# Kernel optimization log

Hardware: AMD Instinct MI355X
Metric: run time of the kernel (lower is better)

Reference implementation:

```python
import jax, jax.numpy as jnp
import numpy as np

B, T, D = 8, 2048, 512
F = 512          # filters (== D due to residual add)
K = 7            # kernel_size
H = 128          # hidden_dim of kernel generator (hard-coded in source)
LN_EPS = 1e-3    # keras LayerNormalization default epsilon


def setup_inputs() -> dict:
    key = jax.random.key(0)
    ks = jax.random.split(key, 8)
    x = jax.random.normal(ks[0], (B, T, D), dtype=jnp.float32)
    # kernel generator: Dense(D->H, relu) then Dense(H->K*F)
    W1 = jax.random.normal(ks[1], (D, H), dtype=jnp.float32) * (1.0 / np.sqrt(D))
    b1 = jnp.zeros((H,), dtype=jnp.float32)
    W2 = jax.random.normal(ks[2], (H, K * F), dtype=jnp.float32) * (1.0 / np.sqrt(H))
    b2 = jnp.zeros((K * F,), dtype=jnp.float32)
    # LayerNorm params
    gamma = jnp.ones((F,), dtype=jnp.float32)
    beta = jnp.zeros((F,), dtype=jnp.float32)
    return {"x": x, "W1": W1, "b1": b1, "W2": W2, "b2": b2,
            "gamma": gamma, "beta": beta}


def _dynamic_conv_block(x, W1, b1, W2, b2, gamma, beta):
    # per-token dynamic kernels: [B, T, K, F]
    h = jax.nn.relu(jnp.einsum("btd,dh->bth", x, W1) + b1)
    kernels = (jnp.einsum("bth,hf->btf", h, W2) + b2).reshape(B, T, K, F)
    # extract sliding-window patches (same padding): [B, T, K, D]
    pad = K // 2
    xp = jnp.pad(x, ((0, 0), (pad, pad), (0, 0)))
    patches = jnp.stack([xp[:, i:i + T, :] for i in range(K)], axis=2)
    # per-token conv: contract over window K and input channels D
    conv_out = jnp.einsum("btkd,btkf->btf", patches, kernels)
    # residual + LayerNorm + relu (dropout is identity at inference)
    y = conv_out + x
    mu = jnp.mean(y, axis=-1, keepdims=True)
    var = jnp.mean(jnp.square(y - mu), axis=-1, keepdims=True)
    y = (y - mu) * jax.lax.rsqrt(var + LN_EPS) * gamma + beta
    return jax.nn.relu(y)


def reference(x, W1, b1, W2, b2, gamma, beta):
    return _dynamic_conv_block(x, W1, b1, W2, b2, gamma, beta)
```

## Files before the change

kernel.cpp:

```cpp
#include <hip/hip_runtime.h>

#define NB 8
#define NT 2048
#define ND 512
#define NH 128
#define NF 512
#define NKW 7
#define NTOK (NB*NT)
#define KP 960

typedef float f32x4 __attribute__((ext_vector_type(4)));
typedef __bf16 bf16x8 __attribute__((ext_vector_type(8)));
typedef unsigned short u16;
typedef unsigned int u32;
typedef u16 u16x8 __attribute__((ext_vector_type(8)));

__device__ __forceinline__ u16 f2bf(float f){
  u32 u = __builtin_bit_cast(u32, f);
  return (u16)((u + 0x7fffu + ((u>>16)&1u)) >> 16);
}
__device__ __forceinline__ float bf2f(u16 s){
  u32 u = ((u32)s)<<16;
  return __builtin_bit_cast(float, u);
}
__device__ __forceinline__ void gload_lds16(const void* g, void* l){
  __builtin_amdgcn_global_load_lds(
      (const __attribute__((address_space(1))) void*)g,
      (__attribute__((address_space(3))) void*)l, 16, 0, 0);
}
__device__ __forceinline__ void store16_lds(void* p, const u16 u[8]){
  u32 d0 = (u32)u[0] | ((u32)u[1]<<16);
  u32 d1 = (u32)u[2] | ((u32)u[3]<<16);
  u32 d2 = (u32)u[4] | ((u32)u[5]<<16);
  u32 d3 = (u32)u[6] | ((u32)u[7]<<16);
  int4 vv; vv.x=(int)d0; vv.y=(int)d1; vv.z=(int)d2; vv.w=(int)d3;
  *(int4*)p = vv;
}

__global__ __launch_bounds__(256) void prep_kernel(
    const float* __restrict__ W1, const float* __restrict__ W2,
    const float* __restrict__ b2, u16* __restrict__ W1T, u16* __restrict__ B2T)
{
  int e = blockIdx.x*256 + threadIdx.x;
  if (e < ND*NH){
    int k = e >> 7, h = e & (NH-1);
    W1T[h*ND + k] = f2bf(W1[e]);
  } else if (e < ND*NH + NH*NKW*NF){
    int c = e - ND*NH;
    int h = c / (NKW*NF);
    int col = c - h*(NKW*NF);
    int k = col >> 9, n = col & (NF-1);
    B2T[(size_t)n*KP + k*NH + h] = f2bf(W2[c]);
  } else if (e < ND*NH + NH*NKW*NF + NF*64){
    int c = e - (ND*NH + NH*NKW*NF);
    int n = c >> 6, j = c & 63;
    B2T[(size_t)n*KP + 896 + j] = (j < NKW) ? f2bf(b2[j*NF + n]) : (u16)0;
  }
}

__global__ __launch_bounds__(256) void rowsum_kernel(
    const float* __restrict__ x, float* __restrict__ rs)
{
  int t = blockIdx.x*4 + (threadIdx.x>>6);
  int l = threadIdx.x & 63;
  const float4* p = (const float4*)(x + (size_t)t*ND + l*8);
  float4 a = p[0], b = p[1];
  float s = (a.x+a.y)+(a.z+a.w)+((b.x+b.y)+(b.z+b.w));
  #pragma unroll
  for (int m=1;m<64;m<<=1) s += __shfl_xor(s, m);
  if (l==0) rs[t] = s;
}

__global__ __launch_bounds__(256) void gemm1_kernel(
    const float* __restrict__ x, const u16* __restrict__ W1T,
    const float* __restrict__ b1, u16* __restrict__ hout)
{
  __shared__ __align__(16) u16 At[64*64];
  __shared__ __align__(16) u16 Bt[128*64];
  const int tid = threadIdx.x, w = tid>>6, l = tid&63;
  const int m_base = blockIdx.x*64;
  f32x4 acc[4][2] = {};
  for (int kc=0; kc<8; ++kc){
    if (kc) __syncthreads();
    #pragma unroll
    for (int it=0; it<2; ++it){
      int c = tid + it*256;
      int row = c>>3, slot = c&7;
      const float4* px = (const float4*)(x + (size_t)(m_base+row)*ND + kc*64 + slot*8);
      float4 a = px[0], b = px[1];
      u16 u[8] = {f2bf(a.x),f2bf(a.y),f2bf(a.z),f2bf(a.w),
                  f2bf(b.x),f2bf(b.y),f2bf(b.z),f2bf(b.w)};
      int byte = row*128 + ((slot*16) ^ ((row&7)<<4));
      store16_lds((char*)At + byte, u);
    }
    #pragma unroll
    for (int i=0;i<4;++i){
      int rowbase = i*32 + w*8;
      char* ldsbase = (char*)Bt + rowbase*128;
      int n = rowbase + (l>>3);
      const char* g = (const char*)W1T + (size_t)n*1024 + kc*128
                      + (((l&7)*16) ^ (((l>>3)&7)<<4));
      gload_lds16(g, ldsbase);
    }
    asm volatile("s_waitcnt vmcnt(0)" ::: "memory");
    __syncthreads();
    #pragma unroll
    for (int kk=0; kk<2; ++kk){
      bf16x8 af[4], bfr[2];
      #pragma unroll
      for (int mi=0;mi<4;++mi){
        int row = mi*16 + (l&15);
        int byte = row*128 + (((kk*64)+((l>>4)*16)) ^ ((row&7)<<4));
        af[mi] = *(const bf16x8*)((const char*)At + byte);
      }
      #pragma unroll
      for (int ni=0;ni<2;++ni){
        int row = w*32 + ni*16 + (l&15);
        int byte = row*128 + (((kk*64)+((l>>4)*16)) ^ ((row&7)<<4));
        bfr[ni] = *(const bf16x8*)((const char*)Bt + byte);
      }
      #pragma unroll
      for (int mi=0;mi<4;++mi)
        #pragma unroll
        for (int ni=0;ni<2;++ni)
          acc[mi][ni] = __builtin_amdgcn_mfma_f32_16x16x32_bf16(af[mi], bfr[ni], acc[mi][ni], 0,0,0);
    }
  }
  #pragma unroll
  for (int ni=0;ni<2;++ni){
    int n = w*32 + ni*16 + (l&15);
    float bias = b1[n];
    #pragma unroll
    for (int mi=0;mi<4;++mi){
      #pragma unroll
      for (int r=0;r<4;++r){
        int m = mi*16 + (l>>4)*4 + r;
        float v = fmaxf(acc[mi][ni][r] + bias, 0.f);
        hout[(size_t)(m_base+m)*NH + n] = f2bf(v);
      }
    }
  }
}

__global__ __launch_bounds__(512) void gemm2_kernel(
    const float* __restrict__ x, const u16* __restrict__ hbuf,
    const u16* __restrict__ B2T, const float* __restrict__ rs,
    const float* __restrict__ gamma, const float* __restrict__ beta,
    float* __restrict__ out)
{
  __shared__ __align__(16) u16 At[64*64];
  __shared__ __align__(16) u16 Bt[512*64];
  __shared__ float s_lds[64][8];
  __shared__ float g_lds[512], be_lds[512];
  __shared__ float red_s[64][8], red_q[64][8];
  __shared__ float mu_lds[64], rstd_lds[64];

  const int tid = threadIdx.x, w = tid>>6, l = tid&63;
  const int m_base = blockIdx.x*64;

  g_lds[tid] = gamma[tid];
  be_lds[tid] = beta[tid];
  {
    int row = tid>>3, k = tid&7;
    float v = 0.f;
    if (k < NKW){
      int tg = m_base + row;
      int ti = tg & (NT-1);
      int idx = ti + k - 3;
      if (idx >= 0 && idx < NT) v = rs[(tg & ~(NT-1)) + idx];
    }
    s_lds[row][k] = v;
  }

  f32x4 acc[4][4] = {};
  for (int kc=0; kc<15; ++kc){
    __syncthreads();
    {
      int row = tid>>3, slot = tid&7;
      u16 u[8];
      if (kc < 14){
        float sv = s_lds[row][kc>>1];
        u16x8 hv = *(const u16x8*)(hbuf + (size_t)(m_base+row)*NH + (kc&1)*64 + slot*8);
        #pragma unroll
        for (int j=0;j<8;++j) u[j] = f2bf(bf2f(hv[j])*sv);
      } else {
        #pragma unroll
        for (int j=0;j<8;++j){
          int e2 = slot*8+j;
          float v = (e2<NKW)? s_lds[row][e2] : 0.f;
          u[j] = f2bf(v);
        }
      }
      int byte = row*128 + ((slot*16) ^ ((row&7)<<4));
      store16_lds((char*)At + byte, u);
    }
    #pragma unroll
    for (int i=0;i<8;++i){
      int rowbase = i*64 + w*8;
      char* ldsbase = (char*)Bt + rowbase*128;
      int n = rowbase + (l>>3);
      const char* g = (const char*)B2T + (size_t)n*(KP*2) + kc*128
                      + (((l&7)*16) ^ (((l>>3)&7)<<4));
      gload_lds16(g, ldsbase);
    }
    asm volatile("s_waitcnt vmcnt(0)" ::: "memory");
    __syncthreads();
    #pragma unroll
    for (int kk=0; kk<2; ++kk){
      bf16x8 af[4], bfr[4];
      #pragma unroll
      for (int mi=0;mi<4;++mi){
        int row = mi*16 + (l&15);
        int byte = row*128 + (((kk*64)+((l>>4)*16)) ^ ((row&7)<<4));
        af[mi] = *(const bf16x8*)((const char*)At + byte);
      }
      #pragma unroll
      for (int ni=0;ni<4;++ni){
        int row = w*64 + ni*16 + (l&15);
        int byte = row*128 + (((kk*64)+((l>>4)*16)) ^ ((row&7)<<4));
        bfr[ni] = *(const bf16x8*)((const char*)Bt + byte);
      }
      #pragma unroll
      for (int mi=0;mi<4;++mi)
        #pragma unroll
        for (int ni=0;ni<4;++ni)
          acc[mi][ni] = __builtin_amdgcn_mfma_f32_16x16x32_bf16(af[mi], bfr[ni], acc[mi][ni], 0,0,0);
    }
  }
  #pragma unroll
  for (int mi=0;mi<4;++mi){
    #pragma unroll
    for (int r=0;r<4;++r){
      int m = mi*16 + (l>>4)*4 + r;
      int tg = m_base + m;
      float ps=0.f, pq=0.f;
      #pragma unroll
      for (int ni=0;ni<4;++ni){
        int n = w*64 + ni*16 + (l&15);
        float v = acc[mi][ni][r] + x[(size_t)tg*ND + n];
        acc[mi][ni][r] = v;
        ps += v; pq += v*v;
      }
      #pragma unroll
      for (int msk=1; msk<16; msk<<=1){ ps += __shfl_xor(ps,msk); pq += __shfl_xor(pq,msk); }
      if ((l&15)==0){ red_s[m][w]=ps; red_q[m][w]=pq; }
    }
  }
  __syncthreads();
  if (tid < 64){
    float ssum=0.f, sq=0.f;
    #pragma unroll
    for (int ww=0; ww<8; ++ww){ ssum += red_s[tid][ww]; sq += red_q[tid][ww]; }
    float mu = ssum * (1.0f/ND);
    float var = sq*(1.0f/ND) - mu*mu;
    mu_lds[tid] = mu;
    rstd_lds[tid] = rsqrtf(var + 1e-3f);
  }
  __syncthreads();
  #pragma unroll
  for (int mi=0;mi<4;++mi){
    #pragma unroll
    for (int r=0;r<4;++r){
      int m = mi*16 + (l>>4)*4 + r;
      int tg = m_base + m;
      float mu = mu_lds[m], rstd = rstd_lds[m];
      #pragma unroll
      for (int ni=0;ni<4;++ni){
        int n = w*64 + ni*16 + (l&15);
        float v = (acc[mi][ni][r]-mu)*rstd*g_lds[n] + be_lds[n];
        out[(size_t)tg*ND + n] = fmaxf(v, 0.f);
      }
    }
  }
}

extern "C" void kernel_launch(void* const* d_in, const int* in_sizes, int n_in,
                              void* d_out, int out_size, void* d_ws, size_t ws_size,
                              hipStream_t stream)
{
  (void)in_sizes; (void)n_in; (void)out_size; (void)ws_size;
  const float* x     = (const float*)d_in[0];
  const float* W1    = (const float*)d_in[1];
  const float* b1    = (const float*)d_in[2];
  const float* W2    = (const float*)d_in[3];
  const float* b2    = (const float*)d_in[4];
  const float* gamma = (const float*)d_in[5];
  const float* beta  = (const float*)d_in[6];
  float* out = (float*)d_out;

  char* ws = (char*)d_ws;
  u16*   W1T  = (u16*)(ws);
  u16*   B2T  = (u16*)(ws + 131072);
  float* rs   = (float*)(ws + 131072 + 983040);
  u16*   hbuf = (u16*)(ws + 131072 + 983040 + 65536);

  prep_kernel<<<2176, 256, 0, stream>>>(W1, W2, b2, W1T, B2T);
  rowsum_kernel<<<NTOK/4, 256, 0, stream>>>(x, rs);
  gemm1_kernel<<<NTOK/64, 256, 0, stream>>>(x, W1T, b1, hbuf);
  gemm2_kernel<<<NTOK/64, 512, 0, stream>>>(x, hbuf, B2T, rs, gamma, beta, out);
}
```

Baseline: 148.2 us.

## Fuse rowsum into gemm1, register-prefetch B operands, double-buffer A tiles

```diff
diff --git a/kernel.cpp b/kernel.cpp
--- a/kernel.cpp
+++ b/kernel.cpp
@@ -1,12 +1,9 @@
 #include <hip/hip_runtime.h>
 
-#define NB 8
 #define NT 2048
 #define ND 512
 #define NH 128
-#define NF 512
 #define NKW 7
-#define NTOK (NB*NT)
 #define KP 960
 
 typedef float f32x4 __attribute__((ext_vector_type(4)));
@@ -22,11 +19,6 @@
 __device__ __forceinline__ float bf2f(u16 s){
   u32 u = ((u32)s)<<16;
   return __builtin_bit_cast(float, u);
-}
-__device__ __forceinline__ void gload_lds16(const void* g, void* l){
-  __builtin_amdgcn_global_load_lds(
-      (const __attribute__((address_space(1))) void*)g,
-      (__attribute__((address_space(3))) void*)l, 16, 0, 0);
 }
 __device__ __forceinline__ void store16_lds(void* p, const u16 u[8]){
   u32 d0 = (u32)u[0] | ((u32)u[1]<<16);
@@ -41,97 +33,136 @@
     const float* __restrict__ W1, const float* __restrict__ W2,
     const float* __restrict__ b2, u16* __restrict__ W1T, u16* __restrict__ B2T)
 {
-  int e = blockIdx.x*256 + threadIdx.x;
-  if (e < ND*NH){
-    int k = e >> 7, h = e & (NH-1);
-    W1T[h*ND + k] = f2bf(W1[e]);
-  } else if (e < ND*NH + NH*NKW*NF){
-    int c = e - ND*NH;
-    int h = c / (NKW*NF);
-    int col = c - h*(NKW*NF);
-    int k = col >> 9, n = col & (NF-1);
-    B2T[(size_t)n*KP + k*NH + h] = f2bf(W2[c]);
-  } else if (e < ND*NH + NH*NKW*NF + NF*64){
-    int c = e - (ND*NH + NH*NKW*NF);
-    int n = c >> 6, j = c & 63;
-    B2T[(size_t)n*KP + 896 + j] = (j < NKW) ? f2bf(b2[j*NF + n]) : (u16)0;
-  }
-}
-
-__global__ __launch_bounds__(256) void rowsum_kernel(
-    const float* __restrict__ x, float* __restrict__ rs)
+  __shared__ float T[64][65];
+  const int b = blockIdx.x, tid = threadIdx.x;
+  if (b < 16){
+    const int d0 = (b>>1)*64, h0 = (b&1)*64;
+    #pragma unroll
+    for (int r=0;r<16;++r){
+      int idx=r*256+tid; int dl=idx>>6, hl=idx&63;
+      T[dl][hl] = W1[(size_t)(d0+dl)*NH + h0+hl];
+    }
+    __syncthreads();
+    #pragma unroll
+    for (int r=0;r<16;++r){
+      int idx=r*256+tid; int hl=idx>>6, dl=idx&63;
+      W1T[(size_t)(h0+hl)*ND + d0+dl] = f2bf(T[dl][hl]);
+    }
+  } else if (b < 128){
+    const int bb = b-16;
+    const int h0 = (bb&1)*64, c0 = (bb>>1)*64;
+    #pragma unroll
+    for (int r=0;r<16;++r){
+      int idx=r*256+tid; int hl=idx>>6, cl=idx&63;
+      T[hl][cl] = W2[(size_t)(h0+hl)*(NKW*ND) + c0+cl];
+    }
+    __syncthreads();
+    #pragma unroll
+    for (int r=0;r<16;++r){
+      int idx=r*256+tid; int cl=idx>>6, hl=idx&63;
+      int c = c0+cl; int n = c & (ND-1), k = c >> 9;
+      B2T[(size_t)n*KP + k*NH + h0+hl] = f2bf(T[hl][cl]);
+    }
+  } else {
+    const int bb = b-128;
+    #pragma unroll
+    for (int r=0;r<16;++r){
+      int idx = bb*4096 + r*256 + tid;
+      int n = idx>>6, j = idx&63;
+      B2T[(size_t)n*KP + 896 + j] = (j<NKW)? f2bf(b2[(size_t)j*ND+n]) : (u16)0;
+    }
+  }
+}
+
+__device__ __forceinline__ void loadB2(const char* B2T, int kc, int w, int l,
+                                       bf16x8 (*bf)[4]){
+  #pragma unroll
+  for (int kk=0;kk<2;++kk)
+    #pragma unroll
+    for (int ni=0;ni<4;++ni){
+      int rowB = w*64 + ni*16 + (l&15);
+      bf[kk][ni] = *(const bf16x8*)(B2T + (size_t)rowB*(KP*2) + kc*128 + kk*64 + (l>>4)*16);
+    }
+}
+__device__ __forceinline__ void loadB1(const char* W1T, int kc, int w, int l,
+                                       bf16x8 (*bf)[2]){
+  #pragma unroll
+  for (int kk=0;kk<2;++kk)
+    #pragma unroll
+    for (int ni=0;ni<2;++ni){
+      int rowB = w*32 + ni*16 + (l&15);
+      bf[kk][ni] = *(const bf16x8*)(W1T + (size_t)rowB*(ND*2) + kc*128 + kk*64 + (l>>4)*16);
+    }
+}
+
+__global__ __launch_bounds__(256,2) void gemm1_kernel(
+    const float* __restrict__ x, const u16* __restrict__ W1T,
+    const float* __restrict__ b1, u16* __restrict__ hout, float* __restrict__ rs)
 {
-  int t = blockIdx.x*4 + (threadIdx.x>>6);
-  int l = threadIdx.x & 63;
-  const float4* p = (const float4*)(x + (size_t)t*ND + l*8);
-  float4 a = p[0], b = p[1];
-  float s = (a.x+a.y)+(a.z+a.w)+((b.x+b.y)+(b.z+b.w));
-  #pragma unroll
-  for (int m=1;m<64;m<<=1) s += __shfl_xor(s, m);
-  if (l==0) rs[t] = s;
-}
-
-__global__ __launch_bounds__(256) void gemm1_kernel(
-    const float* __restrict__ x, const u16* __restrict__ W1T,
-    const float* __restrict__ b1, u16* __restrict__ hout)
-{
-  __shared__ __align__(16) u16 At[64*64];
-  __shared__ __align__(16) u16 Bt[128*64];
+  __shared__ __align__(16) u16 At[2][32*64];
   const int tid = threadIdx.x, w = tid>>6, l = tid&63;
-  const int m_base = blockIdx.x*64;
-  f32x4 acc[4][2] = {};
-  for (int kc=0; kc<8; ++kc){
-    if (kc) __syncthreads();
-    #pragma unroll
-    for (int it=0; it<2; ++it){
-      int c = tid + it*256;
-      int row = c>>3, slot = c&7;
-      const float4* px = (const float4*)(x + (size_t)(m_base+row)*ND + kc*64 + slot*8);
-      float4 a = px[0], b = px[1];
-      u16 u[8] = {f2bf(a.x),f2bf(a.y),f2bf(a.z),f2bf(a.w),
-                  f2bf(b.x),f2bf(b.y),f2bf(b.z),f2bf(b.w)};
-      int byte = row*128 + ((slot*16) ^ ((row&7)<<4));
-      store16_lds((char*)At + byte, u);
-    }
-    #pragma unroll
-    for (int i=0;i<4;++i){
-      int rowbase = i*32 + w*8;
-      char* ldsbase = (char*)Bt + rowbase*128;
-      int n = rowbase + (l>>3);
-      const char* g = (const char*)W1T + (size_t)n*1024 + kc*128
-                      + (((l&7)*16) ^ (((l>>3)&7)<<4));
-      gload_lds16(g, ldsbase);
-    }
-    asm volatile("s_waitcnt vmcnt(0)" ::: "memory");
-    __syncthreads();
-    #pragma unroll
-    for (int kk=0; kk<2; ++kk){
-      bf16x8 af[4], bfr[2];
-      #pragma unroll
-      for (int mi=0;mi<4;++mi){
-        int row = mi*16 + (l&15);
-        int byte = row*128 + (((kk*64)+((l>>4)*16)) ^ ((row&7)<<4));
-        af[mi] = *(const bf16x8*)((const char*)At + byte);
-      }
-      #pragma unroll
-      for (int ni=0;ni<2;++ni){
-        int row = w*32 + ni*16 + (l&15);
-        int byte = row*128 + (((kk*64)+((l>>4)*16)) ^ ((row&7)<<4));
-        bfr[ni] = *(const bf16x8*)((const char*)Bt + byte);
-      }
-      #pragma unroll
-      for (int mi=0;mi<4;++mi)
+  const int m_base = blockIdx.x*32;
+  const int row = tid>>3, slot = tid&7;
+  const float* xrow = x + (size_t)(m_base+row)*ND + slot*8;
+  float rsum = 0.f;
+  f32x4 acc[2][2] = {};
+  bf16x8 bufA[2][2], bufB[2][2];
+
+  auto stageA = [&](u16* dst, const float4& p0, const float4& p1){
+    rsum += (p0.x+p0.y)+(p0.z+p0.w)+((p1.x+p1.y)+(p1.z+p1.w));
+    u16 u[8] = {f2bf(p0.x),f2bf(p0.y),f2bf(p0.z),f2bf(p0.w),
+                f2bf(p1.x),f2bf(p1.y),f2bf(p1.z),f2bf(p1.w)};
+    int byte = row*128 + ((slot*16) ^ ((row&7)<<4));
+    store16_lds((char*)dst + byte, u);
+  };
+
+  float4 c0 = *(const float4*)(xrow);
+  float4 c1 = *(const float4*)(xrow+4);
+  loadB1((const char*)W1T, 0, w, l, bufA);
+  stageA(At[0], c0, c1);
+  __syncthreads();
+
+  #pragma unroll
+  for (int kc=0;kc<8;++kc){
+    bf16x8 (*bc)[2] = (kc&1)? bufB : bufA;
+    bf16x8 (*bn)[2] = (kc&1)? bufA : bufB;
+    float4 n0, n1;
+    if (kc<7){
+      n0 = *(const float4*)(xrow + (kc+1)*64);
+      n1 = *(const float4*)(xrow + (kc+1)*64 + 4);
+      loadB1((const char*)W1T, kc+1, w, l, bn);
+    }
+    const char* curA = (const char*)At[kc&1];
+    #pragma unroll
+    for (int kk=0;kk<2;++kk){
+      bf16x8 af[2];
+      #pragma unroll
+      for (int mi=0;mi<2;++mi){
+        int r2 = mi*16 + (l&15);
+        int byte = r2*128 + (((kk*64)+((l>>4)*16)) ^ ((r2&7)<<4));
+        af[mi] = *(const bf16x8*)(curA + byte);
+      }
+      #pragma unroll
+      for (int mi=0;mi<2;++mi)
         #pragma unroll
         for (int ni=0;ni<2;++ni)
-          acc[mi][ni] = __builtin_amdgcn_mfma_f32_16x16x32_bf16(af[mi], bfr[ni], acc[mi][ni], 0,0,0);
-    }
-  }
+          acc[mi][ni] = __builtin_amdgcn_mfma_f32_16x16x32_bf16(af[mi], bc[kk][ni], acc[mi][ni],0,0,0);
+    }
+    if (kc<7){
+      stageA(At[(kc&1)^1], n0, n1);
+      __syncthreads();
+    }
+  }
+  rsum += __shfl_xor(rsum,1);
+  rsum += __shfl_xor(rsum,2);
+  rsum += __shfl_xor(rsum,4);
+  if ((tid&7)==0) rs[m_base+row] = rsum;
   #pragma unroll
   for (int ni=0;ni<2;++ni){
     int n = w*32 + ni*16 + (l&15);
     float bias = b1[n];
     #pragma unroll
-    for (int mi=0;mi<4;++mi){
+    for (int mi=0;mi<2;++mi){
       #pragma unroll
       for (int r=0;r<4;++r){
         int m = mi*16 + (l>>4)*4 + r;
@@ -142,91 +173,88 @@
   }
 }
 
-__global__ __launch_bounds__(512) void gemm2_kernel(
+__global__ __launch_bounds__(512,2) void gemm2_kernel(
     const float* __restrict__ x, const u16* __restrict__ hbuf,
     const u16* __restrict__ B2T, const float* __restrict__ rs,
     const float* __restrict__ gamma, const float* __restrict__ beta,
     float* __restrict__ out)
 {
-  __shared__ __align__(16) u16 At[64*64];
-  __shared__ __align__(16) u16 Bt[512*64];
+  __shared__ __align__(16) u16 At[2][64*64];
   __shared__ float s_lds[64][8];
-  __shared__ float g_lds[512], be_lds[512];
   __shared__ float red_s[64][8], red_q[64][8];
   __shared__ float mu_lds[64], rstd_lds[64];
 
   const int tid = threadIdx.x, w = tid>>6, l = tid&63;
   const int m_base = blockIdx.x*64;
-
-  g_lds[tid] = gamma[tid];
-  be_lds[tid] = beta[tid];
+  const int row = tid>>3, slot = tid&7;
+
   {
-    int row = tid>>3, k = tid&7;
+    int rr = tid>>3, k = tid&7;
     float v = 0.f;
     if (k < NKW){
-      int tg = m_base + row;
+      int tg = m_base + rr;
       int ti = tg & (NT-1);
       int idx = ti + k - 3;
       if (idx >= 0 && idx < NT) v = rs[(tg & ~(NT-1)) + idx];
     }
-    s_lds[row][k] = v;
-  }
+    s_lds[rr][k] = v;
+  }
+  u16x8 hv_e = *(const u16x8*)(hbuf + (size_t)(m_base+row)*NH + slot*8);
+  u16x8 hv_o = *(const u16x8*)(hbuf + (size_t)(m_base+row)*NH + 64 + slot*8);
+
+  bf16x8 bufA[2][4], bufB[2][4];
+  loadB2((const char*)B2T, 0, w, l, bufA);
+
+  auto stageA = [&](u16* dst, int kc2){
+    u16 u[8];
+    if (kc2 < 14){
+      float sv = s_lds[row][kc2>>1];
+      u16x8 hv = (kc2&1)? hv_o : hv_e;
+      #pragma unroll
+      for (int j=0;j<8;++j) u[j] = f2bf(bf2f(hv[j])*sv);
+    } else {
+      #pragma unroll
+      for (int j=0;j<8;++j){
+        int e2 = slot*8+j;
+        u[j] = (e2<NKW)? f2bf(s_lds[row][e2]) : (u16)0;
+      }
+    }
+    int byte = row*128 + ((slot*16) ^ ((row&7)<<4));
+    store16_lds((char*)dst + byte, u);
+  };
+
+  __syncthreads();
+  stageA(At[0], 0);
+  __syncthreads();
 
   f32x4 acc[4][4] = {};
-  for (int kc=0; kc<15; ++kc){
-    __syncthreads();
-    {
-      int row = tid>>3, slot = tid&7;
-      u16 u[8];
-      if (kc < 14){
-        float sv = s_lds[row][kc>>1];
-        u16x8 hv = *(const u16x8*)(hbuf + (size_t)(m_base+row)*NH + (kc&1)*64 + slot*8);
-        #pragma unroll
-        for (int j=0;j<8;++j) u[j] = f2bf(bf2f(hv[j])*sv);
-      } else {
-        #pragma unroll
-        for (int j=0;j<8;++j){
-          int e2 = slot*8+j;
-          float v = (e2<NKW)? s_lds[row][e2] : 0.f;
-          u[j] = f2bf(v);
-        }
-      }
-      int byte = row*128 + ((slot*16) ^ ((row&7)<<4));
-      store16_lds((char*)At + byte, u);
-    }
-    #pragma unroll
-    for (int i=0;i<8;++i){
-      int rowbase = i*64 + w*8;
-      char* ldsbase = (char*)Bt + rowbase*128;
-      int n = rowbase + (l>>3);
-      const char* g = (const char*)B2T + (size_t)n*(KP*2) + kc*128
-                      + (((l&7)*16) ^ (((l>>3)&7)<<4));
-      gload_lds16(g, ldsbase);
-    }
-    asm volatile("s_waitcnt vmcnt(0)" ::: "memory");
-    __syncthreads();
-    #pragma unroll
-    for (int kk=0; kk<2; ++kk){
-      bf16x8 af[4], bfr[4];
+  #pragma unroll
+  for (int kc=0;kc<15;++kc){
+    bf16x8 (*bc)[4] = (kc&1)? bufB : bufA;
+    bf16x8 (*bn)[4] = (kc&1)? bufA : bufB;
+    if (kc<14) loadB2((const char*)B2T, kc+1, w, l, bn);
+    const char* curA = (const char*)At[kc&1];
+    #pragma unroll
+    for (int kk=0;kk<2;++kk){
+      bf16x8 af[4];
       #pragma unroll
       for (int mi=0;mi<4;++mi){
-        int row = mi*16 + (l&15);
-        int byte = row*128 + (((kk*64)+((l>>4)*16)) ^ ((row&7)<<4));
-        af[mi] = *(const bf16x8*)((const char*)At + byte);
-      }
-      #pragma unroll
-      for (int ni=0;ni<4;++ni){
-        int row = w*64 + ni*16 + (l&15);
-        int byte = row*128 + (((kk*64)+((l>>4)*16)) ^ ((row&7)<<4));
-        bfr[ni] = *(const bf16x8*)((const char*)Bt + byte);
+        int r2 = mi*16 + (l&15);
+        int byte = r2*128 + (((kk*64)+((l>>4)*16)) ^ ((r2&7)<<4));
+        af[mi] = *(const bf16x8*)(curA + byte);
       }
       #pragma unroll
       for (int mi=0;mi<4;++mi)
         #pragma unroll
         for (int ni=0;ni<4;++ni)
-          acc[mi][ni] = __builtin_amdgcn_mfma_f32_16x16x32_bf16(af[mi], bfr[ni], acc[mi][ni], 0,0,0);
-    }
-  }
+          acc[mi][ni] = __builtin_amdgcn_mfma_f32_16x16x32_bf16(af[mi], bc[kk][ni], acc[mi][ni],0,0,0);
+    }
+    if (kc<14){
+      stageA(At[(kc&1)^1], kc+1);
+      __syncthreads();
+    }
+  }
+
   #pragma unroll
   for (int mi=0;mi<4;++mi){
     #pragma unroll
@@ -257,6 +285,12 @@
     rstd_lds[tid] = rsqrtf(var + 1e-3f);
   }
   __syncthreads();
+  float gv[4], bv[4];
+  #pragma unroll
+  for (int ni=0;ni<4;++ni){
+    int n = w*64 + ni*16 + (l&15);
+    gv[ni] = gamma[n]; bv[ni] = beta[n];
+  }
   #pragma unroll
   for (int mi=0;mi<4;++mi){
     #pragma unroll
@@ -267,7 +301,7 @@
       #pragma unroll
       for (int ni=0;ni<4;++ni){
         int n = w*64 + ni*16 + (l&15);
-        float v = (acc[mi][ni][r]-mu)*rstd*g_lds[n] + be_lds[n];
+        float v = (acc[mi][ni][r]-mu)*rstd*gv[ni] + bv[ni];
         out[(size_t)tg*ND + n] = fmaxf(v, 0.f);
       }
     }
@@ -294,8 +328,7 @@
   float* rs   = (float*)(ws + 131072 + 983040);
   u16*   hbuf = (u16*)(ws + 131072 + 983040 + 65536);
 
-  prep_kernel<<<2176, 256, 0, stream>>>(W1, W2, b2, W1T, B2T);
-  rowsum_kernel<<<NTOK/4, 256, 0, stream>>>(x, rs);
-  gemm1_kernel<<<NTOK/64, 256, 0, stream>>>(x, W1T, b1, hbuf);
-  gemm2_kernel<<<NTOK/64, 512, 0, stream>>>(x, hbuf, B2T, rs, gamma, beta, out);
-}
+  prep_kernel<<<136, 256, 0, stream>>>(W1, W2, b2, W1T, B2T);
+  gemm1_kernel<<<512, 256, 0, stream>>>(x, W1T, b1, hbuf, rs);
+  gemm2_kernel<<<256, 512, 0, stream>>>(x, hbuf, B2T, rs, gamma, beta, out);
+}
```

New measurement: 142.1 us. 4.1% less time.
